# Performance work log

Hardware: AMD Instinct MI355X
Metric: run time of the kernel (lower is better)

Reference implementation:

```python
import jax, jax.numpy as jnp
import numpy as np

N_QUBITS = 10
N_QLAYERS = 2
EMBED = 1024
B, S = 16, 1024
DIM = 2 ** N_QUBITS


def _apply_rx(state, theta, w, n):
    # state: [N, 2^n] complex; RX(theta) on wire w (wire 0 = most significant bit)
    nb = state.shape[0]
    left, right = 2 ** w, 2 ** (n - 1 - w)
    psi = state.reshape(nb, left, 2, right)
    t = jnp.asarray(theta, jnp.float32) * 0.5
    c, s = jnp.cos(t), jnp.sin(t)
    if c.ndim == 1:  # per-sample angles
        c, s = c[:, None, None], s[:, None, None]
    a0, a1 = psi[:, :, 0, :], psi[:, :, 1, :]
    n0 = c * a0 - 1j * s * a1
    n1 = -1j * s * a0 + c * a1
    return jnp.stack([n0, n1], axis=2).reshape(nb, -1)


def _apply_cnot(state, c, t, n):
    # CNOT with control wire c, target wire t
    psi = state.reshape((-1,) + (2,) * n)
    ctrl_ax, tgt_ax = c + 1, t + 1
    psi0, psi1 = jnp.split(psi, 2, axis=ctrl_ax)
    psi1 = jnp.flip(psi1, axis=tgt_ax)
    return jnp.concatenate([psi0, psi1], axis=ctrl_ax).reshape(state.shape)


def setup_inputs() -> dict:
    key = jax.random.key(0)
    ks = jax.random.split(key, 6)
    s1 = 1.0 / np.sqrt(EMBED)
    s2 = 1.0 / np.sqrt(N_QUBITS)
    return {
        "x": jax.random.normal(ks[0], (B, S, EMBED), jnp.float32),
        "W1": jax.random.uniform(ks[1], (N_QUBITS, EMBED), jnp.float32, -s1, s1),
        "b1": jax.random.uniform(ks[2], (N_QUBITS,), jnp.float32, -s1, s1),
        "qweights": jax.random.uniform(ks[3], (N_QLAYERS, N_QUBITS), jnp.float32, 0.0, 2.0 * np.pi),
        "W2": jax.random.uniform(ks[4], (EMBED, N_QUBITS), jnp.float32, -s2, s2),
        "b2": jax.random.uniform(ks[5], (EMBED,), jnp.float32, -s2, s2),
    }


def reference(x, W1, b1, qweights, W2, b2):
    n = N_QUBITS
    # linear_1
    ang = (jnp.einsum('bse,qe->bsq', x, W1) + b1).reshape(-1, n)  # [N, n]
    N = ang.shape[0]
    # |0...0> batched state vector
    state = jnp.zeros((N, DIM), jnp.complex64).at[:, 0].set(1.0)
    # AngleEmbedding: RX(ang[:, w]) on each wire
    for w in range(n):
        state = _apply_rx(state, ang[:, w], w, n)
    # BasicEntanglerLayers: RX rotations + CNOT ring per layer
    for l in range(N_QLAYERS):
        for w in range(n):
            state = _apply_rx(state, qweights[l, w], w, n)
        if n == 2:
            state = _apply_cnot(state, 0, 1, n)
        elif n > 2:
            for i in range(n):
                state = _apply_cnot(state, i, (i + 1) % n, n)
    # <Z_w> = sum_idx probs[idx] * (1 - 2*bit_w(idx))
    probs = jnp.real(state * jnp.conj(state))  # [N, 2^n]
    idx = jnp.arange(DIM)
    bits = (idx[:, None] >> (n - 1 - jnp.arange(n))[None, :]) & 1
    signs = (1 - 2 * bits).astype(jnp.float32)  # [2^n, n]
    ev = (probs @ signs).reshape(x.shape[0], x.shape[1], n)  # [B, S, n]
    # linear_2
    return jnp.einsum('bsq,eq->bse', ev, W2) + b2
```

## Files before the change

### kernel.cpp

```cpp
#include <hip/hip_runtime.h>

#define NQ 10
#define EMBED 1024
#define ROWS_PER_BLOCK 32
#define BLOCK 512


constexpr int kPop(int x) { int c = 0; for (int i = 0; i < 10; ++i) c += (x >> i) & 1; return c; }

constexpr int sigma_map(int a) {
    int b = 0;
    for (int i = 0; i < 9; ++i) b |= (((a >> i) & 1) ^ ((a >> (i + 1)) & 1)) << i;
    b |= (((a >> 9) & 1) ^ ((a >> 0) & 1) ^ ((a >> 1) & 1)) << 9;
    return b;
}

#define MAXT 40
struct Terms {
    int nt[NQ];
    int vm[NQ];
    int um[NQ];
    unsigned short tm[NQ][MAXT];
    unsigned short sm[NQ][MAXT];
    float sg[NQ][MAXT];
};

constexpr Terms gen_terms() {
    Terms t{};
    int inv_e[NQ] = {};
    for (int a = 0; a < 1024; ++a) {
        const int s = sigma_map(a);
        for (int q = 0; q < NQ; ++q) if (s == (1 << q)) inv_e[q] = a;
    }
    for (int q = 0; q < NQ; ++q) {
        const int u = inv_e[q];
        int v = 0;
        for (int w = 0; w < NQ; ++w) if ((u >> w) & 1) v ^= inv_e[w];
        t.um[q] = u; t.vm[q] = v;
        int n = 0;
        int S = 0;
        while (true) {
            int T = (((S >> 0) ^ (S >> 9)) & 1)
                  | ((((S >> 0) ^ (S >> 1) ^ (S >> 9)) & 1) << 1);
            for (int j = 2; j < 10; ++j) T |= ((((S >> (j - 1)) ^ (S >> j)) & 1) << j);
            if ((T & ~v) == 0) {
                const int p = kPop(T) + kPop(S);
                if (!(p & 1)) {
                    t.tm[q][n] = (unsigned short)T;
                    t.sm[q][n] = (unsigned short)S;
                    t.sg[q][n] = (p & 2) ? -1.f : 1.f;
                    ++n;
                }
            }
            if (S == u) break;
            S = (S - u) & u;
        }
        t.nt[q] = n;
    }
    return t;
}

constexpr Terms TT = gen_terms();

template <int CTRL, int RM>
__device__ __forceinline__ float dppadd(float v) {
    const int s = __builtin_amdgcn_update_dpp(0, __float_as_int(v), CTRL, RM, 0xF, true);
    return v + __int_as_float(s);
}
__device__ __forceinline__ float red32(float v) {
    v = dppadd<0xB1,  0xF>(v);
    v = dppadd<0x4E,  0xF>(v);
    v = dppadd<0x141, 0xF>(v);
    v = dppadd<0x140, 0xF>(v);
    v = dppadd<0x142, 0xA>(v);
    return v;
}

#define FMA1(ACC, XV, WW)                 \
    ACC = fmaf((XV).x, (WW).x, ACC);      \
    ACC = fmaf((XV).y, (WW).y, ACC);      \
    ACC = fmaf((XV).z, (WW).z, ACC);      \
    ACC = fmaf((XV).w, (WW).w, ACC);

extern "C" __global__ __launch_bounds__(BLOCK, 4)
void ffq_kernel(const float* __restrict__ x, const float* __restrict__ W1,
                const float* __restrict__ b1, const float* __restrict__ qw,
                const float* __restrict__ W2, const float* __restrict__ b2,
                float* __restrict__ out)
{
    __shared__ float sW1[NQ * EMBED];
    __shared__ float sCA[ROWS_PER_BLOCK][11];
    __shared__ float sSA[ROWS_PER_BLOCK][11];
    __shared__ float sEVv[ROWS_PER_BLOCK][11];

    const int tid  = threadIdx.x;
    const int lane = tid & 63;
    const int wv   = tid >> 6;
    const int o    = lane & 31;
    const int g    = lane >> 5;
    const int block0 = blockIdx.x * ROWS_PER_BLOCK;
    const int rloc0  = wv * 4 + g * 2;

    const float4* xr0 = (const float4*)(x + (size_t)(block0 + rloc0) * EMBED);
    const float4* xr1 = (const float4*)(x + (size_t)(block0 + rloc0 + 1) * EMBED);
    float4 xv0[8], xv1[8];
    #pragma unroll
    for (int k = 0; k < 8; ++k) xv0[k] = xr0[k * 32 + o];
    #pragma unroll
    for (int k = 0; k < 8; ++k) xv1[k] = xr1[k * 32 + o];

    {
        const float4* src = (const float4*)W1;
#if __has_builtin(__builtin_amdgcn_global_load_lds)
        typedef const __attribute__((address_space(1))) unsigned int as1_t;
        typedef __attribute__((address_space(3))) unsigned int as3_t;
        float4* dstbase = (float4*)sW1;
        #pragma unroll
        for (int i = 0; i < 5; ++i) {
            const int c = i * 512 + wv * 64;
            __builtin_amdgcn_global_load_lds((as1_t*)(src + c + lane),
                                             (as3_t*)(dstbase + c),
                                             16, 0, 0);
        }
#else
        float4* dst = (float4*)sW1;
        #pragma unroll
        for (int i = 0; i < 5; ++i) dst[tid + BLOCK * i] = src[tid + BLOCK * i];
#endif
    }

    float b1q[NQ];
    #pragma unroll
    for (int w = 0; w < NQ; ++w) b1q[w] = b1[w] + qw[w];

    __syncthreads();

    {
        float acc0[NQ], acc1[NQ];
        #pragma unroll
        for (int q = 0; q < NQ; ++q) { acc0[q] = 0.f; acc1[q] = 0.f; }

        const float4* w1v = (const float4*)sW1;
        #pragma unroll
        for (int k = 0; k < 8; ++k) {
            float4 wA[5];
            #pragma unroll
            for (int q = 0; q < 5; ++q) wA[q] = w1v[q * 256 + k * 32 + o];
            #pragma unroll
            for (int q = 0; q < 5; ++q) {
                FMA1(acc0[q], xv0[k], wA[q]);
                FMA1(acc1[q], xv1[k], wA[q]);
            }
            float4 wB[5];
            #pragma unroll
            for (int q = 0; q < 5; ++q) wB[q] = w1v[(5 + q) * 256 + k * 32 + o];
            #pragma unroll
            for (int q = 0; q < 5; ++q) {
                FMA1(acc0[5 + q], xv0[k], wB[q]);
                FMA1(acc1[5 + q], xv1[k], wB[q]);
            }
        }

        #pragma unroll
        for (int q = 0; q < NQ; ++q) {
            acc0[q] = red32(acc0[q]);
            acc1[q] = red32(acc1[q]);
        }

        if (o == 16) {
            #pragma unroll
            for (int w = 0; w < NQ; ++w) {
                const float A = acc0[w] + b1q[w];
                sCA[rloc0][w] = __cosf(A);
                sSA[rloc0][w] = __sinf(A);
            }
        } else if (o == 17) {
            #pragma unroll
            for (int w = 0; w < NQ; ++w) {
                const float A = acc1[w] + b1q[w];
                sCA[rloc0 + 1][w] = __cosf(A);
                sSA[rloc0 + 1][w] = __sinf(A);
            }
        }
    }

    const int e4 = tid & 255;
    float w2f[40];
    {
        const float4* w2v = (const float4*)(W2 + e4 * 40);
        #pragma unroll
        for (int i = 0; i < 10; ++i) {
            float4 v = w2v[i];
            w2f[4*i+0] = v.x; w2f[4*i+1] = v.y; w2f[4*i+2] = v.z; w2f[4*i+3] = v.w;
        }
    }
    const float4 b2v = ((const float4*)b2)[e4];

    __syncthreads();

    if (lane < ROWS_PER_BLOCK) {
        const int row = lane;
        float ca[NQ], sa[NQ], cb[NQ], sb[NQ];
        #pragma unroll
        for (int w = 0; w < NQ; ++w) {
            ca[w] = sCA[row][w];
            sa[w] = sSA[row][w];
            const float B = qw[NQ + w];
            cb[w] = __cosf(B); sb[w] = __sinf(B);
        }
        #define EVQ(QC) do {                                                      \
            float ev = 0.f;                                                       \
            _Pragma("unroll")                                                     \
            for (int k = 0; k < TT.nt[QC]; ++k) {                                 \
                float P = TT.sg[QC][k];                                           \
                _Pragma("unroll")                                                 \
                for (int w = 0; w < NQ; ++w) {                                    \
                    if ((TT.vm[QC] >> w) & 1) P *= ((TT.tm[QC][k] >> w) & 1) ? sa[w] : ca[w]; \
                    if ((TT.um[QC] >> w) & 1) P *= ((TT.sm[QC][k] >> w) & 1) ? sb[w] : cb[w]; \
                }                                                                 \
                ev += P;                                                          \
            }                                                                     \
            sEVv[row][QC] = ev;                                                   \
        } while (0)
        switch (wv) {
            case 0: EVQ(0); break;
            case 1: EVQ(9); break;
            case 2: EVQ(7); break;
            case 3: EVQ(8); break;
            case 4: EVQ(5); EVQ(6); break;
            case 5: EVQ(3); EVQ(4); break;
            case 6: EVQ(1); EVQ(2); break;
            default: break;
        }
        #undef EVQ
    }

    __syncthreads();

    const int r0 = (tid >> 8) * 16;
    #pragma unroll
    for (int r = 0; r < 16; ++r) {
        const int rr = r0 + r;
        float evr[NQ];
        #pragma unroll
        for (int q = 0; q < NQ; ++q) evr[q] = sEVv[rr][q];
        float o0 = b2v.x, o1 = b2v.y, o2 = b2v.z, o3 = b2v.w;
        #pragma unroll
        for (int q = 0; q < NQ; ++q) {
            o0 = fmaf(evr[q], w2f[ 0 + q], o0);
            o1 = fmaf(evr[q], w2f[10 + q], o1);
            o2 = fmaf(evr[q], w2f[20 + q], o2);
            o3 = fmaf(evr[q], w2f[30 + q], o3);
        }
        float4 ov = {o0, o1, o2, o3};
        ((float4*)(out + (size_t)(block0 + rr) * EMBED))[e4] = ov;
    }
}

extern "C" void kernel_launch(void* const* d_in, const int* in_sizes, int n_in,
                              void* d_out, int out_size, void* d_ws, size_t ws_size,
                              hipStream_t stream) {
    (void)in_sizes; (void)n_in; (void)d_ws; (void)ws_size; (void)out_size;
    const float* x  = (const float*)d_in[0];
    const float* W1 = (const float*)d_in[1];
    const float* b1 = (const float*)d_in[2];
    const float* qw = (const float*)d_in[3];
    const float* W2 = (const float*)d_in[4];
    const float* b2 = (const float*)d_in[5];
    float* out = (float*)d_out;

    const int total_rows = 16 * 1024;
    dim3 grid(total_rows / ROWS_PER_BLOCK);
    ffq_kernel<<<grid, BLOCK, 0, stream>>>(x, W1, b1, qw, W2, b2, out);
}
```

Measured before the change: 30.89 us.

## Halve block size to 16 rows and 256 threads, rebalance EV work

Shrinks each block to 16 rows and 256 threads, which doubles the grid, and rebalances the per-qubit expectation-value terms across the 4 waves. It drops the direct global-to-LDS load of W1 in favour of a plain copy loop, and moves the x row loads to after the barrier. Per-block LDS use is unchanged at 40KB for W1, but that load is now amortised over half as many rows. The x loads no longer overlap the W1 staging, and waves 3 and above take a heavy serial share of the EV computation.

```diff
diff --git a/kernel.cpp b/kernel.cpp
--- a/kernel.cpp
+++ b/kernel.cpp
@@ -2,8 +2,8 @@
 
 #define NQ 10
 #define EMBED 1024
-#define ROWS_PER_BLOCK 32
-#define BLOCK 512
+#define ROWS_PER_BLOCK 16
+#define BLOCK 256
 
 
 constexpr int kPop(int x) { int c = 0; for (int i = 0; i < 10; ++i) c += (x >> i) & 1; return c; }
@@ -82,7 +82,7 @@
     ACC = fmaf((XV).z, (WW).z, ACC);      \
     ACC = fmaf((XV).w, (WW).w, ACC);
 
-extern "C" __global__ __launch_bounds__(BLOCK, 4)
+extern "C" __global__ __launch_bounds__(BLOCK, 3)
 void ffq_kernel(const float* __restrict__ x, const float* __restrict__ W1,
                 const float* __restrict__ b1, const float* __restrict__ qw,
                 const float* __restrict__ W2, const float* __restrict__ b2,
@@ -101,32 +101,11 @@
     const int block0 = blockIdx.x * ROWS_PER_BLOCK;
     const int rloc0  = wv * 4 + g * 2;
 
-    const float4* xr0 = (const float4*)(x + (size_t)(block0 + rloc0) * EMBED);
-    const float4* xr1 = (const float4*)(x + (size_t)(block0 + rloc0 + 1) * EMBED);
-    float4 xv0[8], xv1[8];
-    #pragma unroll
-    for (int k = 0; k < 8; ++k) xv0[k] = xr0[k * 32 + o];
-    #pragma unroll
-    for (int k = 0; k < 8; ++k) xv1[k] = xr1[k * 32 + o];
-
     {
         const float4* src = (const float4*)W1;
-#if __has_builtin(__builtin_amdgcn_global_load_lds)
-        typedef const __attribute__((address_space(1))) unsigned int as1_t;
-        typedef __attribute__((address_space(3))) unsigned int as3_t;
-        float4* dstbase = (float4*)sW1;
-        #pragma unroll
-        for (int i = 0; i < 5; ++i) {
-            const int c = i * 512 + wv * 64;
-            __builtin_amdgcn_global_load_lds((as1_t*)(src + c + lane),
-                                             (as3_t*)(dstbase + c),
-                                             16, 0, 0);
-        }
-#else
         float4* dst = (float4*)sW1;
         #pragma unroll
-        for (int i = 0; i < 5; ++i) dst[tid + BLOCK * i] = src[tid + BLOCK * i];
-#endif
+        for (int i = 0; i < 10; ++i) dst[tid + BLOCK * i] = src[tid + BLOCK * i];
     }
 
     float b1q[NQ];
@@ -136,6 +115,15 @@
     __syncthreads();
 
     {
+        const float4* xr0 = (const float4*)(x + (size_t)(block0 + rloc0) * EMBED);
+        const float4* xr1 = (const float4*)(x + (size_t)(block0 + rloc0 + 1) * EMBED);
+
+        float4 xv0[8], xv1[8];
+        #pragma unroll
+        for (int k = 0; k < 8; ++k) xv0[k] = xr0[k * 32 + o];
+        #pragma unroll
+        for (int k = 0; k < 8; ++k) xv1[k] = xr1[k * 32 + o];
+
         float acc0[NQ], acc1[NQ];
         #pragma unroll
         for (int q = 0; q < NQ; ++q) { acc0[q] = 0.f; acc1[q] = 0.f; }
@@ -184,17 +172,16 @@
         }
     }
 
-    const int e4 = tid & 255;
     float w2f[40];
     {
-        const float4* w2v = (const float4*)(W2 + e4 * 40);
+        const float4* w2v = (const float4*)(W2 + tid * 40);
         #pragma unroll
         for (int i = 0; i < 10; ++i) {
             float4 v = w2v[i];
             w2f[4*i+0] = v.x; w2f[4*i+1] = v.y; w2f[4*i+2] = v.z; w2f[4*i+3] = v.w;
         }
     }
-    const float4 b2v = ((const float4*)b2)[e4];
+    const float4 b2v = ((const float4*)b2)[tid];
 
     __syncthreads();
 
@@ -225,22 +212,16 @@
         switch (wv) {
             case 0: EVQ(0); break;
             case 1: EVQ(9); break;
-            case 2: EVQ(7); break;
-            case 3: EVQ(8); break;
-            case 4: EVQ(5); EVQ(6); break;
-            case 5: EVQ(3); EVQ(4); break;
-            case 6: EVQ(1); EVQ(2); break;
-            default: break;
+            case 2: EVQ(7); EVQ(8); break;
+            default: EVQ(1); EVQ(2); EVQ(3); EVQ(4); EVQ(5); EVQ(6); break;
         }
         #undef EVQ
     }
 
     __syncthreads();
 
-    const int r0 = (tid >> 8) * 16;
     #pragma unroll
-    for (int r = 0; r < 16; ++r) {
-        const int rr = r0 + r;
+    for (int rr = 0; rr < ROWS_PER_BLOCK; ++rr) {
         float evr[NQ];
         #pragma unroll
         for (int q = 0; q < NQ; ++q) evr[q] = sEVv[rr][q];
@@ -253,7 +234,7 @@
             o3 = fmaf(evr[q], w2f[30 + q], o3);
         }
         float4 ov = {o0, o1, o2, o3};
-        ((float4*)(out + (size_t)(block0 + rr) * EMBED))[e4] = ov;
+        ((float4*)(out + (size_t)(block0 + rr) * EMBED))[tid] = ov;
     }
 }
 
```

Measured after the change: 29.04 us. -6.0%, faster.
